# Performance work log

Measured on AMD Instinct MI355X. Metric: run time of the kernel, lower is better.

## Reference

```python
import jax, jax.numpy as jnp
import numpy as np

N = 50000      # num nodes
E = 1600000    # num edges (before self-loops)
DIN, DH, DOUT = 256, 128, 64


def _gcn_norm(edge_index, num_nodes):
    # Add self-loops, then symmetric normalization 1/sqrt(deg_i * deg_j)
    loop = jnp.arange(num_nodes, dtype=edge_index.dtype)
    src = jnp.concatenate([edge_index[0], loop])  # [E+N]
    dst = jnp.concatenate([edge_index[1], loop])  # [E+N]
    deg = jax.ops.segment_sum(jnp.ones_like(dst, dtype=jnp.float32), dst,
                              num_segments=num_nodes)
    dinv = jnp.where(deg > 0, jax.lax.rsqrt(deg), 0.0)
    norm = dinv[src] * dinv[dst]  # [E+N]
    return src, dst, norm


def _gcn_conv(x, src, dst, norm, W, b, num_nodes):
    h = x @ W                                  # [N, out] dense transform first
    msg = h[src] * norm[:, None]               # gather + scale  [E+N, out]
    out = jax.ops.segment_sum(msg, dst, num_segments=num_nodes)  # scatter-add
    return out + b


def reference(x, edge_index, W1, b1, W2, b2):
    num_nodes = x.shape[0]
    src, dst, norm = _gcn_norm(edge_index, num_nodes)
    h = _gcn_conv(x, src, dst, norm, W1, b1, num_nodes)
    h = jax.nn.relu(h)
    # dropout(p=0.5) is identity in eval mode
    out = _gcn_conv(h, src, dst, norm, W2, b2, num_nodes)
    return out


def setup_inputs() -> dict:
    key = jax.random.key(0)
    ks = jax.random.split(key, 6)
    x = jax.random.normal(ks[0], (N, DIN), dtype=jnp.float32)
    edge_index = jax.random.randint(ks[1], (2, E), 0, N, dtype=jnp.int32)
    W1 = jax.random.normal(ks[2], (DIN, DH), dtype=jnp.float32) * (1.0 / np.sqrt(DIN))
    b1 = jnp.zeros((DH,), dtype=jnp.float32)
    W2 = jax.random.normal(ks[3], (DH, DOUT), dtype=jnp.float32) * (1.0 / np.sqrt(DH))
    b2 = jnp.zeros((DOUT,), dtype=jnp.float32)
    return {"x": x, "edge_index": edge_index, "W1": W1, "b1": b1, "W2": W2, "b2": b2}
```

## Files before the change

kernel.cpp:

```cpp
#include <hip/hip_runtime.h>

#define DIN 256
#define DH  128
#define DOUT 64
#define BSH  7
#define BNODES 128
#define MAXBUK 400
#define NBLK 512

typedef unsigned int  u32;
typedef unsigned short u16;
typedef __attribute__((ext_vector_type(8))) short bf16x8;
typedef __attribute__((ext_vector_type(4))) float f32x4;

__device__ inline u16 f2bf(float f) {
  u32 u = __float_as_uint(f);
  u32 r = u + 0x7FFF + ((u >> 16) & 1);
  return (u16)(r >> 16);
}
__device__ inline float bf2f_lo(u32 packed) { return __uint_as_float(packed << 16); }
__device__ inline float bf2f_hi(u32 packed) { return __uint_as_float(packed & 0xFFFF0000u); }


__global__ __launch_bounds__(256) void hist_kernel(const int* __restrict__ dst,
    int* __restrict__ counts, int E, int nbuk) {
  __shared__ int h[MAXBUK];
  int tid = threadIdx.x, b = blockIdx.x;
  for (int i = tid; i < nbuk; i += 256) h[i] = 0;
  __syncthreads();
  int ech = (E + NBLK - 1) / NBLK;
  int e0 = b * ech, e1 = min(E, e0 + ech);
  for (int e = e0 + tid; e < e1; e += 256)
    atomicAdd(&h[dst[e] >> BSH], 1);
  __syncthreads();
  for (int i = tid; i < nbuk; i += 256) counts[(size_t)i * NBLK + b] = h[i];
}

__global__ __launch_bounds__(256) void col_scan(int* __restrict__ counts,
    int* __restrict__ colsum, int nbuk) {
  __shared__ int sm[256];
  __shared__ int carry;
  int buk = blockIdx.x, t = threadIdx.x;
  if (t == 0) carry = 0;
  __syncthreads();
  int* row = counts + (size_t)buk * NBLK;
  for (int base = 0; base < NBLK; base += 256) {
    int v = row[base + t];
    sm[t] = v;
    __syncthreads();
    for (int d = 1; d < 256; d <<= 1) {
      int a = (t >= d) ? sm[t - d] : 0;
      __syncthreads();
      sm[t] += a;
      __syncthreads();
    }
    int excl = sm[t] - v + carry;
    row[base + t] = excl;
    __syncthreads();
    if (t == 255) carry = excl + v;
    __syncthreads();
  }
  if (t == 0) colsum[buk] = carry;
}

__global__ __launch_bounds__(256) void scan_block(int* partial, int* total_out, int nb, int n) {
  __shared__ int sm[256];
  __shared__ int carry;
  int t = threadIdx.x;
  if (t == 0) carry = 0;
  __syncthreads();
  for (int base = 0; base < nb; base += 256) {
    int g = base + t;
    int v = (g < nb) ? partial[g] : 0;
    sm[t] = v;
    __syncthreads();
    for (int d = 1; d < 256; d <<= 1) {
      int add = (t >= d) ? sm[t - d] : 0;
      __syncthreads();
      sm[t] += add;
      __syncthreads();
    }
    int excl = sm[t] - v + carry;
    if (g < nb) partial[g] = excl;
    __syncthreads();
    if (t == 255) carry = excl + v;
    __syncthreads();
  }
  if (t == 0) total_out[n] = carry;
}

__global__ __launch_bounds__(256) void scatter_kernel(const int* __restrict__ src,
    const int* __restrict__ dst, const int* __restrict__ counts,
    const int* __restrict__ bb, u32* __restrict__ ebuf, int E, int nbuk) {
  __shared__ int cur[MAXBUK];
  int tid = threadIdx.x, b = blockIdx.x;
  for (int i = tid; i < nbuk; i += 256)
    cur[i] = bb[i] + counts[(size_t)i * NBLK + b];
  __syncthreads();
  int ech = (E + NBLK - 1) / NBLK;
  int e0 = b * ech, e1 = min(E, e0 + ech);
  for (int e = e0 + tid; e < e1; e += 256) {
    int d = dst[e];
    int r = atomicAdd(&cur[d >> BSH], 1);
    ebuf[r] = (u32)src[e] | ((u32)(d & (BNODES - 1)) << 16);
  }
}

__global__ __launch_bounds__(256) void bucket_node_count(const u32* __restrict__ ebuf,
    const int* __restrict__ bb, int* __restrict__ cnt, int N) {
  __shared__ int c[BNODES];
  int b = blockIdx.x, tid = threadIdx.x;
  if (tid < BNODES) c[tid] = 0;
  __syncthreads();
  int e0 = bb[b], e1 = bb[b + 1];
  for (int e = e0 + tid; e < e1; e += 256)
    atomicAdd(&c[ebuf[e] >> 16], 1);
  __syncthreads();
  int node = b * BNODES + tid;
  if (tid < BNODES && node < N) cnt[node] = c[tid];
}

__global__ __launch_bounds__(256) void reduce_chunks(const int* __restrict__ cnt,
                                                     int* __restrict__ partial, int n) {
  int t = threadIdx.x;
  int g = blockIdx.x * 256 + t;
  int v = (g < n) ? cnt[g] : 0;
  #pragma unroll
  for (int o = 32; o > 0; o >>= 1) v += __shfl_down(v, o, 64);
  __shared__ int sm[4];
  if ((t & 63) == 0) sm[t >> 6] = v;
  __syncthreads();
  if (t == 0) partial[blockIdx.x] = sm[0] + sm[1] + sm[2] + sm[3];
}

__global__ __launch_bounds__(256) void scan_chunks(const int* __restrict__ cnt,
    const int* __restrict__ chunkoff, int* __restrict__ rowptr,
    float* __restrict__ dinv, int n) {
  __shared__ int sm[256];
  int t = threadIdx.x, g = blockIdx.x * 256 + t;
  int v = (g < n) ? cnt[g] : 0;
  sm[t] = v;
  __syncthreads();
  for (int d = 1; d < 256; d <<= 1) {
    int add = (t >= d) ? sm[t - d] : 0;
    __syncthreads();
    sm[t] += add;
    __syncthreads();
  }
  if (g < n) {
    rowptr[g] = sm[t] - v + chunkoff[blockIdx.x];
    dinv[g] = rsqrtf((float)(v + 1));
  }
}

__global__ __launch_bounds__(256) void bucket_fill(const u32* __restrict__ ebuf,
    const int* __restrict__ bb, const int* __restrict__ rowptr, int* __restrict__ csr) {
  __shared__ int c[BNODES];
  int b = blockIdx.x, tid = threadIdx.x;
  if (tid < BNODES) c[tid] = 0;
  __syncthreads();
  int e0 = bb[b], e1 = bb[b + 1];
  for (int e = e0 + tid; e < e1; e += 256) {
    u32 p = ebuf[e];
    int nl = p >> 16;
    int r = atomicAdd(&c[nl], 1);
    csr[rowptr[b * BNODES + nl] + r] = (int)(p & 0xFFFFu);
  }
}


__global__ __launch_bounds__(256) void w_prep(const float* __restrict__ W1,
    const float* __restrict__ W2, u16* __restrict__ w1t, u16* __restrict__ w2t) {
  int t = blockIdx.x * 256 + threadIdx.x;
  if (t < DH * DIN) {
    int n = t >> 8, k = t & 255;
    w1t[t] = f2bf(W1[k * DH + n]);
  } else {
    int t2 = t - DH * DIN;
    int n = t2 >> 7, k = t2 & 127;
    w2t[t2] = f2bf(W2[k * DOUT + n]);
  }
}


__global__ __launch_bounds__(256) void gemm1_mfma(const float* __restrict__ x,
    const u16* __restrict__ w1t, const float* __restrict__ dinv,
    u16* __restrict__ h1, int M) {
  __shared__ u16 As[64][72];
  __shared__ u16 Bs[128][72];
  const int tid = threadIdx.x;
  const int lane = tid & 63, w = tid >> 6;
  const int row16 = lane & 15, quad = lane >> 4;
  const int rowBase = blockIdx.x * 64;
  f32x4 acc[8];
  #pragma unroll
  for (int nt = 0; nt < 8; ++nt) acc[nt] = (f32x4)(0.f);

  for (int kt = 0; kt < DIN; kt += 64) {
    {
      int r = tid >> 2, kq = tid & 3;
      int grow = rowBase + r;
      #pragma unroll
      for (int i = 0; i < 4; ++i) {
        float4 v = make_float4(0.f, 0.f, 0.f, 0.f);
        if (grow < M) v = *(const float4*)&x[(size_t)grow * DIN + kt + kq * 16 + i * 4];
        u32 lo = (u32)f2bf(v.x) | ((u32)f2bf(v.y) << 16);
        u32 hi = (u32)f2bf(v.z) | ((u32)f2bf(v.w) << 16);
        *(uint2*)&As[r][kq * 16 + i * 4] = make_uint2(lo, hi);
      }
    }
    {
      int n = tid >> 1, half = tid & 1;
      const uint4* s = (const uint4*)&w1t[n * DIN + kt + half * 32];
      uint4* d = (uint4*)&Bs[n][half * 32];
      d[0] = s[0]; d[1] = s[1]; d[2] = s[2]; d[3] = s[3];
    }
    __syncthreads();
    #pragma unroll
    for (int ks = 0; ks < 64; ks += 32) {
      bf16x8 a = *(bf16x8*)&As[w * 16 + row16][ks + quad * 8];
      #pragma unroll
      for (int nt = 0; nt < 8; ++nt) {
        bf16x8 b = *(bf16x8*)&Bs[nt * 16 + row16][ks + quad * 8];
        acc[nt] = __builtin_amdgcn_mfma_f32_16x16x32_bf16(a, b, acc[nt], 0, 0, 0);
      }
    }
    __syncthreads();
  }
  #pragma unroll
  for (int reg = 0; reg < 4; ++reg) {
    int row = rowBase + w * 16 + quad * 4 + reg;
    if (row < M) {
      float s = dinv[row];
      #pragma unroll
      for (int nt = 0; nt < 8; ++nt)
        h1[(size_t)row * DH + nt * 16 + row16] = f2bf(acc[nt][reg] * s);
    }
  }
}


__global__ __launch_bounds__(256) void gemm2_mfma(const u16* __restrict__ g1,
    const u16* __restrict__ w2t, const float* __restrict__ dinv,
    u16* __restrict__ h2, int M) {
  __shared__ u16 As[64][136];
  __shared__ u16 Bs[64][136];
  const int tid = threadIdx.x;
  const int lane = tid & 63, w = tid >> 6;
  const int row16 = lane & 15, quad = lane >> 4;
  const int rowBase = blockIdx.x * 64;
  f32x4 acc[4];
  #pragma unroll
  for (int nt = 0; nt < 4; ++nt) acc[nt] = (f32x4)(0.f);

  #pragma unroll
  for (int i = 0; i < 4; ++i) {
    int flat = i * 256 + tid;
    int r = flat >> 4, c = flat & 15;
    int grow = rowBase + r;
    uint4 v = make_uint4(0, 0, 0, 0);
    if (grow < M) v = *(const uint4*)&g1[(size_t)grow * DH + c * 8];
    *(uint4*)&As[r][c * 8] = v;
  }
  #pragma unroll
  for (int i = 0; i < 4; ++i) {
    int flat = i * 256 + tid;
    int r = flat >> 4, c = flat & 15;
    *(uint4*)&Bs[r][c * 8] = *(const uint4*)&w2t[r * DH + c * 8];
  }
  __syncthreads();
  #pragma unroll
  for (int ks = 0; ks < 128; ks += 32) {
    bf16x8 a = *(bf16x8*)&As[w * 16 + row16][ks + quad * 8];
    #pragma unroll
    for (int nt = 0; nt < 4; ++nt) {
      bf16x8 b = *(bf16x8*)&Bs[nt * 16 + row16][ks + quad * 8];
      acc[nt] = __builtin_amdgcn_mfma_f32_16x16x32_bf16(a, b, acc[nt], 0, 0, 0);
    }
  }
  #pragma unroll
  for (int reg = 0; reg < 4; ++reg) {
    int row = rowBase + w * 16 + quad * 4 + reg;
    if (row < M) {
      float s = dinv[row];
      #pragma unroll
      for (int nt = 0; nt < 4; ++nt)
        h2[(size_t)row * DOUT + nt * 16 + row16] = f2bf(acc[nt][reg] * s);
    }
  }
}


__global__ __launch_bounds__(256) void aggregate1(const u16* __restrict__ h,
    const int* __restrict__ rowptr, const int* __restrict__ csr,
    const float* __restrict__ dinv, const float* __restrict__ bias,
    u16* __restrict__ out, int n) {
  int lane = threadIdx.x & 63;
  int node = blockIdx.x * 4 + (threadIdx.x >> 6);
  if (node >= n) return;
  node = __builtin_amdgcn_readfirstlane(node);
  float di = dinv[node];
  int c0 = lane * 2;
  u32 w0 = *(const u32*)&h[(size_t)node * DH + c0];
  float ax = bf2f_lo(w0), ay = bf2f_hi(w0);
  int p = rowptr[node], pe = rowptr[node + 1];
  for (; p + 16 <= pe; p += 16) {
    int s[16];
    #pragma unroll
    for (int j = 0; j < 16; ++j) s[j] = csr[p + j];
    #pragma unroll
    for (int j = 0; j < 16; ++j) {
      u32 w = *(const u32*)&h[(size_t)s[j] * DH + c0];
      ax += bf2f_lo(w); ay += bf2f_hi(w);
    }
  }
  for (; p + 4 <= pe; p += 4) {
    int s[4];
    #pragma unroll
    for (int j = 0; j < 4; ++j) s[j] = csr[p + j];
    #pragma unroll
    for (int j = 0; j < 4; ++j) {
      u32 w = *(const u32*)&h[(size_t)s[j] * DH + c0];
      ax += bf2f_lo(w); ay += bf2f_hi(w);
    }
  }
  for (; p < pe; ++p) {
    u32 w = *(const u32*)&h[(size_t)csr[p] * DH + c0];
    ax += bf2f_lo(w); ay += bf2f_hi(w);
  }
  ax = fmaxf(fmaf(ax, di, bias[c0]), 0.f);
  ay = fmaxf(fmaf(ay, di, bias[c0 + 1]), 0.f);
  u32 pk = (u32)f2bf(ax) | ((u32)f2bf(ay) << 16);
  *(u32*)&out[(size_t)node * DH + c0] = pk;
}

__global__ __launch_bounds__(256) void aggregate2(const u16* __restrict__ h,
    const int* __restrict__ rowptr, const int* __restrict__ csr,
    const float* __restrict__ dinv, const float* __restrict__ bias,
    float* __restrict__ out, int n) {
  int lane = threadIdx.x & 63;
  int node = blockIdx.x * 4 + (threadIdx.x >> 6);
  if (node >= n) return;
  node = __builtin_amdgcn_readfirstlane(node);
  float di = dinv[node];
  float a = __uint_as_float((u32)h[(size_t)node * DOUT + lane] << 16);
  int p = rowptr[node], pe = rowptr[node + 1];
  for (; p + 16 <= pe; p += 16) {
    int s[16];
    #pragma unroll
    for (int j = 0; j < 16; ++j) s[j] = csr[p + j];
    #pragma unroll
    for (int j = 0; j < 16; ++j)
      a += __uint_as_float((u32)h[(size_t)s[j] * DOUT + lane] << 16);
  }
  for (; p + 4 <= pe; p += 4) {
    int s[4];
    #pragma unroll
    for (int j = 0; j < 4; ++j) s[j] = csr[p + j];
    #pragma unroll
    for (int j = 0; j < 4; ++j)
      a += __uint_as_float((u32)h[(size_t)s[j] * DOUT + lane] << 16);
  }
  for (; p < pe; ++p)
    a += __uint_as_float((u32)h[(size_t)csr[p] * DOUT + lane] << 16);
  out[(size_t)node * DOUT + lane] = fmaf(a, di, bias[lane]);
}


extern "C" void kernel_launch(void* const* d_in, const int* in_sizes, int n_in,
                              void* d_out, int out_size, void* d_ws, size_t ws_size,
                              hipStream_t stream) {
  const float* x  = (const float*)d_in[0];
  const int*   ei = (const int*)d_in[1];
  const float* W1 = (const float*)d_in[2];
  const float* b1 = (const float*)d_in[3];
  const float* W2 = (const float*)d_in[4];
  const float* b2 = (const float*)d_in[5];
  float* out = (float*)d_out;

  const int N = in_sizes[0] / DIN;
  const int E = in_sizes[1] / 2;
  const int* src = ei;
  const int* dst = ei + E;
  const int NB = (N + 255) / 256;
  const int nbuk = (N + BNODES - 1) / BNODES;

  char* ws = (char*)d_ws;
  size_t o = 0;
  auto alloc = [&](size_t bytes) { size_t r = o; o += (bytes + 511) & ~(size_t)511; return r; };
  size_t colsum_o  = alloc((size_t)(nbuk + 1) * 4);
  size_t counts_o  = alloc((size_t)nbuk * NBLK * 4);
  size_t rowptr_o  = alloc((size_t)(N + 1) * 4);
  size_t partial_o = alloc((size_t)NB * 4);
  size_t dinv_o    = alloc((size_t)N * 4);
  size_t cnt_o     = alloc((size_t)N * 4);
  size_t w1t_o     = alloc((size_t)DH * DIN * 2);
  size_t w2t_o     = alloc((size_t)DOUT * DH * 2);
  size_t csr_o     = alloc((size_t)E * 4);
  size_t h1_o      = alloc((size_t)N * DH * 2);
  size_t g1_o      = alloc((size_t)N * DH * 2);
  size_t h2_o      = h1_o;
  size_t ebuf_o    = g1_o;

  int*   colsum  = (int*)(ws + colsum_o);
  int*   counts  = (int*)(ws + counts_o);
  int*   rowptr  = (int*)(ws + rowptr_o);
  int*   partial = (int*)(ws + partial_o);
  float* dinv    = (float*)(ws + dinv_o);
  int*   cnt     = (int*)(ws + cnt_o);
  u16*   w1t     = (u16*)(ws + w1t_o);
  u16*   w2t     = (u16*)(ws + w2t_o);
  int*   csr     = (int*)(ws + csr_o);
  u16*   h1      = (u16*)(ws + h1_o);
  u16*   g1      = (u16*)(ws + g1_o);
  u16*   h2      = (u16*)(ws + h2_o);
  u32*   ebuf    = (u32*)(ws + ebuf_o);

  w_prep<<<(DH * DIN + DOUT * DH) / 256, 256, 0, stream>>>(W1, W2, w1t, w2t);
  hist_kernel<<<NBLK, 256, 0, stream>>>(dst, counts, E, nbuk);
  col_scan<<<nbuk, 256, 0, stream>>>(counts, colsum, nbuk);
  scan_block<<<1, 256, 0, stream>>>(colsum, colsum, nbuk, nbuk);
  scatter_kernel<<<NBLK, 256, 0, stream>>>(src, dst, counts, colsum, ebuf, E, nbuk);
  bucket_node_count<<<nbuk, 256, 0, stream>>>(ebuf, colsum, cnt, N);
  reduce_chunks<<<NB, 256, 0, stream>>>(cnt, partial, N);
  scan_block<<<1, 256, 0, stream>>>(partial, rowptr, NB, N);
  scan_chunks<<<NB, 256, 0, stream>>>(cnt, partial, rowptr, dinv, N);
  bucket_fill<<<nbuk, 256, 0, stream>>>(ebuf, colsum, rowptr, csr);

  gemm1_mfma<<<(N + 63) / 64, 256, 0, stream>>>(x, w1t, dinv, h1, N);
  aggregate1<<<(N + 3) / 4, 256, 0, stream>>>(h1, rowptr, csr, dinv, b1, g1, N);
  gemm2_mfma<<<(N + 63) / 64, 256, 0, stream>>>(g1, w2t, dinv, h2, N);
  aggregate2<<<(N + 3) / 4, 256, 0, stream>>>(h2, rowptr, csr, dinv, b2, out, N);
}
```

Before: 247.1 us.

## Split each wavefront across multiple neighbor rows with 16-byte gathers in aggregation

New measurement: 244.2 us. About the same (-1.2%).

```diff
diff --git a/kernel.cpp b/kernel.cpp
--- a/kernel.cpp
+++ b/kernel.cpp
@@ -295,75 +295,158 @@
     const int* __restrict__ rowptr, const int* __restrict__ csr,
     const float* __restrict__ dinv, const float* __restrict__ bias,
     u16* __restrict__ out, int n) {
-  int lane = threadIdx.x & 63;
+  const int lane = threadIdx.x & 63;
+  const int sub = lane >> 4;
+  const int l16 = lane & 15;
   int node = blockIdx.x * 4 + (threadIdx.x >> 6);
   if (node >= n) return;
   node = __builtin_amdgcn_readfirstlane(node);
-  float di = dinv[node];
-  int c0 = lane * 2;
-  u32 w0 = *(const u32*)&h[(size_t)node * DH + c0];
-  float ax = bf2f_lo(w0), ay = bf2f_hi(w0);
-  int p = rowptr[node], pe = rowptr[node + 1];
-  for (; p + 16 <= pe; p += 16) {
-    int s[16];
-    #pragma unroll
-    for (int j = 0; j < 16; ++j) s[j] = csr[p + j];
-    #pragma unroll
-    for (int j = 0; j < 16; ++j) {
-      u32 w = *(const u32*)&h[(size_t)s[j] * DH + c0];
-      ax += bf2f_lo(w); ay += bf2f_hi(w);
-    }
-  }
-  for (; p + 4 <= pe; p += 4) {
-    int s[4];
-    #pragma unroll
-    for (int j = 0; j < 4; ++j) s[j] = csr[p + j];
-    #pragma unroll
-    for (int j = 0; j < 4; ++j) {
-      u32 w = *(const u32*)&h[(size_t)s[j] * DH + c0];
-      ax += bf2f_lo(w); ay += bf2f_hi(w);
-    }
-  }
-  for (; p < pe; ++p) {
-    u32 w = *(const u32*)&h[(size_t)csr[p] * DH + c0];
-    ax += bf2f_lo(w); ay += bf2f_hi(w);
-  }
-  ax = fmaxf(fmaf(ax, di, bias[c0]), 0.f);
-  ay = fmaxf(fmaf(ay, di, bias[c0 + 1]), 0.f);
-  u32 pk = (u32)f2bf(ax) | ((u32)f2bf(ay) << 16);
-  *(u32*)&out[(size_t)node * DH + c0] = pk;
+  const float di = dinv[node];
+
+  float a[8];
+  {
+    uint4 v = *(const uint4*)&h[(size_t)node * DH + l16 * 8];
+    float ms = (sub == 0) ? 1.f : 0.f;
+    a[0] = ms * bf2f_lo(v.x); a[1] = ms * bf2f_hi(v.x);
+    a[2] = ms * bf2f_lo(v.y); a[3] = ms * bf2f_hi(v.y);
+    a[4] = ms * bf2f_lo(v.z); a[5] = ms * bf2f_hi(v.z);
+    a[6] = ms * bf2f_lo(v.w); a[7] = ms * bf2f_hi(v.w);
+  }
+
+  int p = rowptr[node];
+  const int pe = rowptr[node + 1];
+  while (p < pe) {
+    int g = p + lane;
+    int si = (g < pe) ? csr[g] : 0;
+    int rem = pe - p; if (rem > 64) rem = 64;
+    int t = 0;
+    for (; t + 16 <= rem; t += 16) {
+      #pragma unroll
+      for (int q = 0; q < 4; ++q) {
+        int idx = __shfl(si, t + q * 4 + sub, 64);
+        uint4 v = *(const uint4*)&h[(size_t)idx * DH + l16 * 8];
+        a[0] += bf2f_lo(v.x); a[1] += bf2f_hi(v.x);
+        a[2] += bf2f_lo(v.y); a[3] += bf2f_hi(v.y);
+        a[4] += bf2f_lo(v.z); a[5] += bf2f_hi(v.z);
+        a[6] += bf2f_lo(v.w); a[7] += bf2f_hi(v.w);
+      }
+    }
+    for (; t < rem; t += 4) {
+      int e = t + sub;
+      int idx = __shfl(si, e & 63, 64);
+      uint4 v = *(const uint4*)&h[(size_t)idx * DH + l16 * 8];
+      float m = (e < rem) ? 1.f : 0.f;
+      a[0] = fmaf(m, bf2f_lo(v.x), a[0]); a[1] = fmaf(m, bf2f_hi(v.x), a[1]);
+      a[2] = fmaf(m, bf2f_lo(v.y), a[2]); a[3] = fmaf(m, bf2f_hi(v.y), a[3]);
+      a[4] = fmaf(m, bf2f_lo(v.z), a[4]); a[5] = fmaf(m, bf2f_hi(v.z), a[5]);
+      a[6] = fmaf(m, bf2f_lo(v.w), a[6]); a[7] = fmaf(m, bf2f_hi(v.w), a[7]);
+    }
+    p += 64;
+  }
+
+  #pragma unroll
+  for (int i = 0; i < 8; ++i) {
+    a[i] += __shfl_xor(a[i], 16, 64);
+    a[i] += __shfl_xor(a[i], 32, 64);
+  }
+
+  if (sub == 0) {
+    const int c0 = l16 * 8;
+    float4 b0 = *(const float4*)&bias[c0];
+    float4 b1 = *(const float4*)&bias[c0 + 4];
+    float r0 = fmaxf(fmaf(a[0], di, b0.x), 0.f);
+    float r1 = fmaxf(fmaf(a[1], di, b0.y), 0.f);
+    float r2 = fmaxf(fmaf(a[2], di, b0.z), 0.f);
+    float r3 = fmaxf(fmaf(a[3], di, b0.w), 0.f);
+    float r4 = fmaxf(fmaf(a[4], di, b1.x), 0.f);
+    float r5 = fmaxf(fmaf(a[5], di, b1.y), 0.f);
+    float r6 = fmaxf(fmaf(a[6], di, b1.z), 0.f);
+    float r7 = fmaxf(fmaf(a[7], di, b1.w), 0.f);
+    u32 pk[4];
+    pk[0] = (u32)f2bf(r0) | ((u32)f2bf(r1) << 16);
+    pk[1] = (u32)f2bf(r2) | ((u32)f2bf(r3) << 16);
+    pk[2] = (u32)f2bf(r4) | ((u32)f2bf(r5) << 16);
+    pk[3] = (u32)f2bf(r6) | ((u32)f2bf(r7) << 16);
+    *(uint4*)&out[(size_t)node * DH + c0] = *(uint4*)pk;
+  }
 }
 
 __global__ __launch_bounds__(256) void aggregate2(const u16* __restrict__ h,
     const int* __restrict__ rowptr, const int* __restrict__ csr,
     const float* __restrict__ dinv, const float* __restrict__ bias,
     float* __restrict__ out, int n) {
-  int lane = threadIdx.x & 63;
+  const int lane = threadIdx.x & 63;
+  const int sub = lane >> 3;
+  const int l8 = lane & 7;
   int node = blockIdx.x * 4 + (threadIdx.x >> 6);
   if (node >= n) return;
   node = __builtin_amdgcn_readfirstlane(node);
-  float di = dinv[node];
-  float a = __uint_as_float((u32)h[(size_t)node * DOUT + lane] << 16);
-  int p = rowptr[node], pe = rowptr[node + 1];
-  for (; p + 16 <= pe; p += 16) {
-    int s[16];
-    #pragma unroll
-    for (int j = 0; j < 16; ++j) s[j] = csr[p + j];
-    #pragma unroll
-    for (int j = 0; j < 16; ++j)
-      a += __uint_as_float((u32)h[(size_t)s[j] * DOUT + lane] << 16);
-  }
-  for (; p + 4 <= pe; p += 4) {
-    int s[4];
-    #pragma unroll
-    for (int j = 0; j < 4; ++j) s[j] = csr[p + j];
-    #pragma unroll
-    for (int j = 0; j < 4; ++j)
-      a += __uint_as_float((u32)h[(size_t)s[j] * DOUT + lane] << 16);
-  }
-  for (; p < pe; ++p)
-    a += __uint_as_float((u32)h[(size_t)csr[p] * DOUT + lane] << 16);
-  out[(size_t)node * DOUT + lane] = fmaf(a, di, bias[lane]);
+  const float di = dinv[node];
+
+  float a[8];
+  {
+    uint4 v = *(const uint4*)&h[(size_t)node * DOUT + l8 * 8];
+    float ms = (sub == 0) ? 1.f : 0.f;
+    a[0] = ms * bf2f_lo(v.x); a[1] = ms * bf2f_hi(v.x);
+    a[2] = ms * bf2f_lo(v.y); a[3] = ms * bf2f_hi(v.y);
+    a[4] = ms * bf2f_lo(v.z); a[5] = ms * bf2f_hi(v.z);
+    a[6] = ms * bf2f_lo(v.w); a[7] = ms * bf2f_hi(v.w);
+  }
+
+  int p = rowptr[node];
+  const int pe = rowptr[node + 1];
+  while (p < pe) {
+    int g = p + lane;
+    int si = (g < pe) ? csr[g] : 0;
+    int rem = pe - p; if (rem > 64) rem = 64;
+    int t = 0;
+    for (; t + 32 <= rem; t += 32) {
+      #pragma unroll
+      for (int q = 0; q < 4; ++q) {
+        int idx = __shfl(si, t + q * 8 + sub, 64);
+        uint4 v = *(const uint4*)&h[(size_t)idx * DOUT + l8 * 8];
+        a[0] += bf2f_lo(v.x); a[1] += bf2f_hi(v.x);
+        a[2] += bf2f_lo(v.y); a[3] += bf2f_hi(v.y);
+        a[4] += bf2f_lo(v.z); a[5] += bf2f_hi(v.z);
+        a[6] += bf2f_lo(v.w); a[7] += bf2f_hi(v.w);
+      }
+    }
+    for (; t < rem; t += 8) {
+      int e = t + sub;
+      int idx = __shfl(si, e & 63, 64);
+      uint4 v = *(const uint4*)&h[(size_t)idx * DOUT + l8 * 8];
+      float m = (e < rem) ? 1.f : 0.f;
+      a[0] = fmaf(m, bf2f_lo(v.x), a[0]); a[1] = fmaf(m, bf2f_hi(v.x), a[1]);
+      a[2] = fmaf(m, bf2f_lo(v.y), a[2]); a[3] = fmaf(m, bf2f_hi(v.y), a[3]);
+      a[4] = fmaf(m, bf2f_lo(v.z), a[4]); a[5] = fmaf(m, bf2f_hi(v.z), a[5]);
+      a[6] = fmaf(m, bf2f_lo(v.w), a[6]); a[7] = fmaf(m, bf2f_hi(v.w), a[7]);
+    }
+    p += 64;
+  }
+
+  #pragma unroll
+  for (int i = 0; i < 8; ++i) {
+    a[i] += __shfl_xor(a[i], 8, 64);
+    a[i] += __shfl_xor(a[i], 16, 64);
+    a[i] += __shfl_xor(a[i], 32, 64);
+  }
+
+  if (sub == 0) {
+    const int c0 = l8 * 8;
+    float4 b0 = *(const float4*)&bias[c0];
+    float4 b1 = *(const float4*)&bias[c0 + 4];
+    float4 r0, r1;
+    r0.x = fmaf(a[0], di, b0.x);
+    r0.y = fmaf(a[1], di, b0.y);
+    r0.z = fmaf(a[2], di, b0.z);
+    r0.w = fmaf(a[3], di, b0.w);
+    r1.x = fmaf(a[4], di, b1.x);
+    r1.y = fmaf(a[5], di, b1.y);
+    r1.z = fmaf(a[6], di, b1.z);
+    r1.w = fmaf(a[7], di, b1.w);
+    *(float4*)&out[(size_t)node * DOUT + c0] = r0;
+    *(float4*)&out[(size_t)node * DOUT + c0 + 4] = r1;
+  }
 }
 
 
```
